# Kernel tuning notes

Hardware: AMD Instinct MI355X
Metric: run time of the kernel (lower is better)

## Reference

```python
import jax, jax.numpy as jnp
import numpy as np

B, P, N, E = 4, 4, 4096, 512
QKV_DIM, HEADS = 512, 8
DH = QKV_DIM // HEADS
EPS = 1e-12  # F.normalize default eps


def setup_inputs() -> dict:
    key = jax.random.key(0)
    ks = jax.random.split(key, 5)
    s = 1.0 / np.sqrt(E)
    return {
        "x": jax.random.normal(ks[0], (B, P, N, E), dtype=jnp.float32),
        "w_qkv": jax.random.normal(ks[1], (3 * QKV_DIM, E), dtype=jnp.float32) * s,
        "b_qkv": jax.random.normal(ks[2], (3 * QKV_DIM,), dtype=jnp.float32) * 0.01,
        "temperature": jnp.ones((HEADS, 1, 1), dtype=jnp.float32),
        "w_out": jax.random.normal(ks[3], (E, QKV_DIM), dtype=jnp.float32) * (1.0 / np.sqrt(QKV_DIM)),
        "b_out": jax.random.normal(ks[4], (E,), dtype=jnp.float32) * 0.01,
    }


def _l2norm(t):
    # F.normalize(t, dim=-1): t / max(||t||_2, eps)
    n = jnp.sqrt(jnp.sum(t * t, axis=-1, keepdims=True))
    return t / jnp.maximum(n, EPS)


def reference(x, w_qkv, b_qkv, temperature, w_out, b_out):
    b, p, n, _ = x.shape
    qkv = x @ w_qkv.T + b_qkv                      # (b,p,n,3*qkv)
    q, k, v = jnp.split(qkv, 3, axis=-1)
    def to_heads(t):
        # (b,p,n,h*dh) -> (b,p,h,dh,n)  (channels-as-tokens)
        t = t.reshape(b, p, n, HEADS, DH)
        return jnp.transpose(t, (0, 1, 3, 4, 2))
    q, k, v = to_heads(q), to_heads(k), to_heads(v)
    q = _l2norm(q)                                  # normalize over tokens n
    k = _l2norm(k)
    # channel-wise (dh x dh) attention per head, temperature-scaled
    attn = jnp.einsum('bphdn,bphen->bphde', q, k) * temperature  # (b,p,h,dh,dh)
    attn = jax.nn.softmax(attn, axis=-1)
    out = jnp.einsum('bphde,bphen->bphdn', attn, v)               # (b,p,h,dh,n)
    # torch rearrange 'b p h n d -> b p d (h n)' on (b,p,h,dh,n) -> (b,p,n,h*dh)
    out = jnp.transpose(out, (0, 1, 4, 2, 3)).reshape(b, p, n, HEADS * DH)
    return out @ w_out.T + b_out
```

## Files before the change

### kernel.cpp

```cpp
#include <hip/hip_runtime.h>
#include <stdint.h>

typedef unsigned short u16;
typedef __bf16 bf16x8 __attribute__((ext_vector_type(8)));
typedef float f32x4 __attribute__((ext_vector_type(4)));

#define AS1 __attribute__((address_space(1)))
#define AS3 __attribute__((address_space(3)))

__device__ __forceinline__ void gload_lds16(u16* lds_wave_base, const u16* g) {
  __builtin_amdgcn_global_load_lds((AS1 void*)g, (AS3 void*)lds_wave_base, 16, 0, 0);
}

__device__ __forceinline__ u16 f2bf(float f) {
  unsigned int u = __float_as_uint(f);
  u += 0x7fffu + ((u >> 16) & 1u);
  return (u16)(u >> 16);
}
__device__ __forceinline__ float bf2f(u16 h) { return __uint_as_float(((unsigned)h) << 16); }

__global__ void cast_f32_bf16(const float* __restrict__ in, u16* __restrict__ out, int n8) {
  int i = blockIdx.x * blockDim.x + threadIdx.x;
  if (i >= n8) return;
  const float4* p = (const float4*)in + (size_t)i * 2;
  float4 a = p[0], b = p[1];
  uint2 lo, hi;
  lo.x = (unsigned)f2bf(a.x) | ((unsigned)f2bf(a.y) << 16);
  lo.y = (unsigned)f2bf(a.z) | ((unsigned)f2bf(a.w) << 16);
  hi.x = (unsigned)f2bf(b.x) | ((unsigned)f2bf(b.y) << 16);
  hi.y = (unsigned)f2bf(b.z) | ((unsigned)f2bf(b.w) << 16);
  uint2* o = (uint2*)out + (size_t)i * 2;
  o[0] = lo;
  o[1] = hi;
}

__global__ __launch_bounds__(256) void cast_x(const float* __restrict__ x,
                                              u16* __restrict__ xbf,
                                              float* __restrict__ svec) {
  __shared__ float sred[4 * 512];
  const int b = blockIdx.x;
  const int bp = b >> 6;
  const int n0 = (b & 63) * 64;
  const int t = threadIdx.x;
  const int e8 = (t & 63) * 8;
  const int r0 = t >> 6;
  const float* xb = x + ((size_t)(bp * 4096 + n0) * 512) + e8;
  u16* ob = xbf + ((size_t)(bp * 4096 + n0) * 512) + e8;
  float s0 = 0.f, s1 = 0.f, s2 = 0.f, s3 = 0.f, s4 = 0.f, s5 = 0.f, s6 = 0.f, s7 = 0.f;
#pragma unroll 2
  for (int pass = 0; pass < 16; ++pass) {
    const int r = pass * 4 + r0;
    const float* p = xb + (size_t)r * 512;
    float4 v0 = *(const float4*)p;
    float4 v1 = *(const float4*)(p + 4);
    uint2 lo, hi;
    lo.x = (unsigned)f2bf(v0.x) | ((unsigned)f2bf(v0.y) << 16);
    lo.y = (unsigned)f2bf(v0.z) | ((unsigned)f2bf(v0.w) << 16);
    hi.x = (unsigned)f2bf(v1.x) | ((unsigned)f2bf(v1.y) << 16);
    hi.y = (unsigned)f2bf(v1.z) | ((unsigned)f2bf(v1.w) << 16);
    uint2* o = (uint2*)(ob + (size_t)r * 512);
    o[0] = lo;
    o[1] = hi;
    s0 += v0.x; s1 += v0.y; s2 += v0.z; s3 += v0.w;
    s4 += v1.x; s5 += v1.y; s6 += v1.z; s7 += v1.w;
  }
  float* sp = &sred[r0 * 512 + e8];
  sp[0] = s0; sp[1] = s1; sp[2] = s2; sp[3] = s3;
  sp[4] = s4; sp[5] = s5; sp[6] = s6; sp[7] = s7;
  __syncthreads();
  {
    const int e = t * 2;
    float a0 = sred[e] + sred[512 + e] + sred[1024 + e] + sred[1536 + e];
    float a1 = sred[e + 1] + sred[512 + e + 1] + sred[1024 + e + 1] + sred[1536 + e + 1];
    float* sv = svec + (size_t)bp * 512 + e;
    atomicAdd(sv + 0, a0);
    atomicAdd(sv + 1, a1);
  }
}

__global__ __launch_bounds__(256) void transpose_x(const u16* __restrict__ xbf,
                                                   u16* __restrict__ xbfT) {
  __shared__ __align__(16) unsigned sm[128 * 36];
  const int b = blockIdx.x;
  const int bp = b >> 8;
  const int tt = (b >> 2) & 63;
  const int et = b & 3;
  const int t = threadIdx.x;
  const int n0 = tt * 64, e0 = et * 128;
  const int c4 = (t & 31) * 4;
  const int pr = t >> 5;
  const int sw1 = t & 15;
  const u16* ib = xbf + ((size_t)(bp * 4096 + n0) * 512) + e0 + c4;
  uint2 ta[4], tb[4];
#pragma unroll
  for (int jp = 0; jp < 4; ++jp) {
    const int n = (jp * 8 + pr) * 2;
    ta[jp] = *(const uint2*)(ib + (size_t)n * 512);
    tb[jp] = *(const uint2*)(ib + (size_t)(n + 1) * 512);
  }
#pragma unroll
  for (int jp = 0; jp < 4; ++jp) {
    const int npair = jp * 8 + pr;
    const uint2 a = ta[jp], v = tb[jp];
    const int col = (npair & 16) | ((npair ^ sw1) & 15);
    sm[(c4 + 0) * 36 + col] = (a.x & 0xFFFFu) | (v.x << 16);
    sm[(c4 + 1) * 36 + col] = (a.x >> 16) | (v.x & 0xFFFF0000u);
    sm[(c4 + 2) * 36 + col] = (a.y & 0xFFFFu) | (v.y << 16);
    sm[(c4 + 3) * 36 + col] = (a.y >> 16) | (v.y & 0xFFFF0000u);
  }
  __syncthreads();
  u16* otb = xbfT + ((size_t)bp * 512 + e0) * 4096 + n0;
#pragma unroll
  for (int it = 0; it < 4; ++it) {
    const int e = it * 32 + (t >> 3);
    const int g = t & 7;
    const int p4 = g * 4;
    const int sw = (e >> 2) & 15;
    const int base = e * 36 + (p4 & 16) + ((p4 ^ sw) & 12);
    uint4 v = *(const uint4*)&sm[base];
    const int s3 = sw & 3;
    unsigned q0 = v.x, q1 = v.y, q2 = v.z, q3 = v.w;
    if (s3 & 1) {
      unsigned tmp = q0; q0 = q1; q1 = tmp;
      tmp = q2; q2 = q3; q3 = tmp;
    }
    if (s3 & 2) {
      unsigned tmp = q0; q0 = q2; q2 = tmp;
      tmp = q1; q1 = q3; q3 = tmp;
    }
    uint4 o;
    o.x = q0; o.y = q1; o.z = q2; o.w = q3;
    *(uint4*)(otb + (size_t)e * 4096 + g * 8) = o;
  }
}

__global__ __launch_bounds__(256) void transpose_wv(const float* __restrict__ wv,
                                                    u16* __restrict__ wvT) {
  __shared__ __align__(16) u16 sm[128 * 136];
  const int b = blockIdx.x;
  const int r0 = (b >> 2) * 128;
  const int c0 = (b & 3) * 128;
  const int t = threadIdx.x;
  const int rsub = t >> 5, c4 = (t & 31) * 4;
#pragma unroll
  for (int j = 0; j < 16; ++j) {
    const int r = j * 8 + rsub;
    float4 v = *(const float4*)(wv + (size_t)(r0 + r) * 512 + c0 + c4);
    sm[(c4 + 0) * 136 + ((j ^ ((c4 + 0) & 15)) << 3) + rsub] = f2bf(v.x);
    sm[(c4 + 1) * 136 + ((j ^ ((c4 + 1) & 15)) << 3) + rsub] = f2bf(v.y);
    sm[(c4 + 2) * 136 + ((j ^ ((c4 + 2) & 15)) << 3) + rsub] = f2bf(v.z);
    sm[(c4 + 3) * 136 + ((j ^ ((c4 + 3) & 15)) << 3) + rsub] = f2bf(v.w);
  }
  __syncthreads();
#pragma unroll
  for (int j = 0; j < 8; ++j) {
    const int re = j * 16 + (t >> 4);
    const int ct8 = t & 15;
    uint4 v = *(const uint4*)&sm[re * 136 + ((ct8 ^ (re & 15)) << 3)];
    *(uint4*)(wvT + (size_t)(c0 + re) * 512 + r0 + ct8 * 8) = v;
  }
}

template <int MODE>
__global__ __launch_bounds__(256) void gemm5(const u16* __restrict__ gA,
                                             const u16* __restrict__ gB,
                                             const float* __restrict__ bias,
                                             void* __restrict__ gC) {
  __shared__ __align__(16) u16 smem[128 * 136];
  u16* As = smem;
  u16* Bs = smem + 4096;
  const int t = threadIdx.x;
  const int w = t >> 6, l = t & 63;
  const int lrow = l & 15, quad = l >> 4;
  const int wm = (w >> 1) * 64, wn = (w & 1) * 64;
  int m0, n0, bp = 0, kc = 0;
  if (MODE == 0) {
    const int bx = blockIdx.x;
    bp = blockIdx.y;
    kc = bx & 3;
    const int p = bx >> 2;
    int ti, tj;
    if (p < 4) { ti = 0; tj = p; }
    else if (p < 7) { ti = 1; tj = p - 3; }
    else if (p < 9) { ti = 2; tj = p - 5; }
    else { ti = 3; tj = 3; }
    m0 = ti * 128;
    n0 = tj * 128;
  } else if (MODE == 1) {
    const int b = blockIdx.x;
    bp = b >> 5;
    const int tl = b & 31;
    m0 = (tl >> 2) * 128;
    n0 = (tl & 3) * 128;
  } else if (MODE == 2) {
    const int b = blockIdx.x;
    bp = b >> 4;
    const int tl = b & 15;
    m0 = (tl >> 2) * 128;
    n0 = (tl & 3) * 128;
  } else {
    const int b = blockIdx.x;
    const int local = b & 127;
    bp = b >> 7;
    const int j = (local >> 3) & 3;
    const int T = ((local >> 5) << 3) | (local & 7);
    m0 = j * 128;
    n0 = T * 128;
  }
  constexpr int LDA = (MODE == 0) ? 4096 : 512;
  constexpr int LDB = (MODE == 0) ? 4096 : 512;
  const u16* pA = gA;
  const u16* pB = gB;
  if (MODE == 0) {
    pA += (size_t)bp * (512 * 4096);
    pB = pA;
  } else if (MODE == 1) {
    pB += (size_t)bp * (512 * 512);
  } else if (MODE == 2) {
    pA += (size_t)bp * (512 * 512);
  } else {
    pA += (size_t)bp * (512 * 512);
    pB += (size_t)bp * (4096 * 512);
  }
  const int srow = w * 32 + (l >> 2);
  const int scol = (l & 3) * 8;
  const int koff = (MODE == 0) ? kc * 1024 : 0;
  const u16* ga0 = pA + (size_t)(m0 + srow) * LDA + scol + koff;
  const u16* ga1 = ga0 + (size_t)16 * LDA;
  const u16* gb0 = pB + (size_t)(n0 + srow) * LDB + scol + koff;
  const u16* gb1 = gb0 + (size_t)16 * LDB;
  u16* lA0 = &As[w * 1024];
  u16* lA1 = lA0 + 512;
  u16* lB0 = &Bs[w * 1024];
  u16* lB1 = lB0 + 512;

  f32x4 acc[4][4];
#pragma unroll
  for (int mi = 0; mi < 4; ++mi)
#pragma unroll
    for (int ni = 0; ni < 4; ++ni) acc[mi][ni] = (f32x4){0.f, 0.f, 0.f, 0.f};

  constexpr int KLEN = (MODE == 0) ? 1024 : 512;
  constexpr int NPH = (MODE == 1) ? 2 : 1;
#pragma unroll 1
  for (int ph = 0; ph < NPH; ++ph) {
    const size_t boff = (MODE == 1) ? (size_t)ph * 4194304 : 0;
#pragma unroll 1
    for (int k0 = 0; k0 < KLEN; k0 += 32) {
      gload_lds16(lA0, ga0 + k0);
      gload_lds16(lA1, ga1 + k0);
      gload_lds16(lB0, gb0 + boff + k0);
      gload_lds16(lB1, gb1 + boff + k0);
      __syncthreads();
      bf16x8 af[4], bfr[4];
#pragma unroll
      for (int mi = 0; mi < 4; ++mi)
        af[mi] = *(const bf16x8*)&As[(wm + mi * 16 + lrow) * 32 + quad * 8];
#pragma unroll
      for (int ni = 0; ni < 4; ++ni)
        bfr[ni] = *(const bf16x8*)&Bs[(wn + ni * 16 + lrow) * 32 + quad * 8];
#pragma unroll
      for (int mi = 0; mi < 4; ++mi)
#pragma unroll
        for (int ni = 0; ni < 4; ++ni)
          acc[mi][ni] = __builtin_amdgcn_mfma_f32_16x16x32_bf16(af[mi], bfr[ni], acc[mi][ni], 0, 0, 0);
      __syncthreads();
    }
  }

  if (MODE == 0 || MODE == 3) {
    float* gCp;
    if (MODE == 0)
      gCp = (float*)gC + (size_t)(kc * 16 + bp) * 262144;
    else
      gCp = (float*)gC + (size_t)bp * (4096 * 512);
    float* fs = (float*)smem;
#pragma unroll
    for (int half = 0; half < 2; ++half) {
      if (half) __syncthreads();
#pragma unroll
      for (int mi = 0; mi < 4; ++mi) {
        const int mrow_l = wm + mi * 16 + quad * 4;
        float4 bb = {0.f, 0.f, 0.f, 0.f};
        if (MODE == 3) bb = *(const float4*)&bias[(size_t)bp * 512 + m0 + mrow_l];
#pragma unroll
        for (int ni = 0; ni < 4; ++ni) {
          const int ncol_l = wn + ni * 16 + lrow;
          if ((ncol_l >> 6) != half) continue;
          f32x4 v = acc[mi][ni];
          float4 o;
          o.x = v[0] + bb.x;
          o.y = v[1] + bb.y;
          o.z = v[2] + bb.z;
          o.w = v[3] + bb.w;
          *(float4*)&fs[(ncol_l & 63) * 136 + mrow_l] = o;
        }
      }
      __syncthreads();
#pragma unroll
      for (int j2 = 0; j2 < 4; ++j2) {
        const int g = j2 * 256 + t;
        const int r = g >> 4;
        const int c = (g & 15) * 8;
        float4 v0 = *(const float4*)&fs[r * 136 + c];
        float4 v1 = *(const float4*)&fs[r * 136 + c + 4];
        float* yp = gCp + ((size_t)(n0 + half * 64 + r) * 512 + m0 + c);
        *(float4*)yp = v0;
        *(float4*)(yp + 4) = v1;
      }
      if (MODE == 0 && m0 != n0) {
#pragma unroll
        for (int j2 = 0; j2 < 8; ++j2) {
          const int g = j2 * 256 + t;
          const int row = g >> 4;
          const int cg = (g & 15) * 4;
          float4 o;
          o.x = fs[(cg + 0) * 136 + row];
          o.y = fs[(cg + 1) * 136 + row];
          o.z = fs[(cg + 2) * 136 + row];
          o.w = fs[(cg + 3) * 136 + row];
          *(float4*)(gCp + (size_t)(m0 + row) * 512 + n0 + half * 64 + cg) = o;
        }
      }
    }
  } else {
    u16* gCp = (u16*)gC + ((MODE == 1) ? (size_t)bp * 524288 : (size_t)bp * 262144);
#pragma unroll
    for (int mi = 0; mi < 4; ++mi) {
      const int mrow_l = wm + mi * 16 + quad * 4;
#pragma unroll
      for (int ni = 0; ni < 4; ++ni) {
        const int ncol_l = wn + ni * 16 + lrow;
        f32x4 v = acc[mi][ni];
        smem[(mrow_l + 0) * 136 + ncol_l] = f2bf(v[0]);
        smem[(mrow_l + 1) * 136 + ncol_l] = f2bf(v[1]);
        smem[(mrow_l + 2) * 136 + ncol_l] = f2bf(v[2]);
        smem[(mrow_l + 3) * 136 + ncol_l] = f2bf(v[3]);
      }
    }
    __syncthreads();
#pragma unroll
    for (int j = 0; j < 8; ++j) {
      const int g = j * 256 + t;
      const int r = g >> 4;
      const int c = (g & 15) * 8;
      uint4 val = *(const uint4*)&smem[r * 136 + c];
      *(uint4*)(gCp + (size_t)(m0 + r) * 512 + n0 + c) = val;
    }
  }
}

__global__ __launch_bounds__(256) void s4red(const float* __restrict__ Spart,
                                             u16* __restrict__ Shi) {
  const size_t i = ((size_t)blockIdx.x * 256 + threadIdx.x) * 4;
  if (i >= 4194304) return;
  float4 a = *(const float4*)(Spart + i);
  float4 b = *(const float4*)(Spart + 4194304 + i);
  float4 c = *(const float4*)(Spart + 2 * 4194304 + i);
  float4 d = *(const float4*)(Spart + 3 * 4194304 + i);
  float s0 = a.x + b.x + c.x + d.x;
  float s1 = a.y + b.y + c.y + d.y;
  float s2 = a.z + b.z + c.z + d.z;
  float s3 = a.w + b.w + c.w + d.w;
  u16 h0 = f2bf(s0), h1 = f2bf(s1), h2 = f2bf(s2), h3 = f2bf(s3);
  uint2 hp;
  hp.x = (unsigned)h0 | ((unsigned)h1 << 16);
  hp.y = (unsigned)h2 | ((unsigned)h3 << 16);
  *(uint2*)(Shi + i) = hp;
  uint2 lp;
  lp.x = (unsigned)f2bf(s0 - bf2f(h0)) | ((unsigned)f2bf(s1 - bf2f(h1)) << 16);
  lp.y = (unsigned)f2bf(s2 - bf2f(h2)) | ((unsigned)f2bf(s3 - bf2f(h3)) << 16);
  *(uint2*)(Shi + 4194304 + i) = lp;
}

__device__ __forceinline__ void bf8_expand(uint4 v, float* o) {
  o[0] = bf2f((u16)(v.x & 0xffff)); o[1] = bf2f((u16)(v.x >> 16));
  o[2] = bf2f((u16)(v.y & 0xffff)); o[3] = bf2f((u16)(v.y >> 16));
  o[4] = bf2f((u16)(v.z & 0xffff)); o[5] = bf2f((u16)(v.z >> 16));
  o[6] = bf2f((u16)(v.w & 0xffff)); o[7] = bf2f((u16)(v.w >> 16));
}

__global__ __launch_bounds__(512) void softmax_weff2(const u16* __restrict__ P,
                                                     const u16* __restrict__ wqkv,
                                                     const float* __restrict__ b_qkv,
                                                     const float* __restrict__ svec,
                                                     const float* __restrict__ temperature,
                                                     const u16* __restrict__ wout,
                                                     u16* __restrict__ Weff) {
  __shared__ __align__(16) float sattn[64 * 64];
  __shared__ __align__(16) u16 sattnT[64 * 64];
  __shared__ float ub[128], dq[128], rnA[128], bb[128];
  const int blk = blockIdx.x;
  const int bp = blk >> 3, h = blk & 7;
  const int t = threadIdx.x, w = t >> 6, l = t & 63;
  const int lrow = l & 15, quad = l >> 4;

  {
    const int mi = w >> 1;
    const int nip = (w & 1) * 2;
    const u16* arow = P + ((size_t)bp * 1024 + h * 64 + mi * 16 + lrow) * 512;
    const u16* brow0 = wqkv + ((size_t)(512 + h * 64 + nip * 16 + lrow)) * 512;
    const u16* brow1 = brow0 + 16 * 512;
    f32x4 c0 = (f32x4){0.f, 0.f, 0.f, 0.f};
    f32x4 c1 = (f32x4){0.f, 0.f, 0.f, 0.f};
#pragma unroll 1
    for (int ks = 0; ks < 16; ++ks) {
      const int ko = ks * 32 + quad * 8;
      bf16x8 a = *(const bf16x8*)(arow + ko);
      bf16x8 b0 = *(const bf16x8*)(brow0 + ko);
      bf16x8 b1 = *(const bf16x8*)(brow1 + ko);
      c0 = __builtin_amdgcn_mfma_f32_16x16x32_bf16(a, b0, c0, 0, 0, 0);
      c1 = __builtin_amdgcn_mfma_f32_16x16x32_bf16(a, b1, c1, 0, 0, 0);
    }
    const int drow = mi * 16 + quad * 4;
#pragma unroll
    for (int r = 0; r < 4; ++r) {
      sattn[(drow + r) * 64 + nip * 16 + lrow] = c0[r];
      sattn[(drow + r) * 64 + (nip + 1) * 16 + lrow] = c1[r];
    }
  }

  {
    const int rr = t >> 2, sub = t & 3;
    const int c = (rr < 64) ? (h * 64 + rr) : (512 + h * 64 + (rr - 64));
    const u16* prow = P + ((size_t)bp * 1024 + c) * 512 + sub * 128;
    const u16* wrow = wqkv + (size_t)c * 512 + sub * 128;
    const float* sv = svec + (size_t)bp * 512 + sub * 128;
    float accp = 0.f, accu = 0.f;
#pragma unroll 1
    for (int i = 0; i < 128; i += 8) {
      float pf[8], wf[8];
      bf8_expand(*(const uint4*)(prow + i), pf);
      bf8_expand(*(const uint4*)(wrow + i), wf);
      float4 s0 = *(const float4*)(sv + i);
      float4 s1 = *(const float4*)(sv + i + 4);
      accp += pf[0] * wf[0] + pf[1] * wf[1] + pf[2] * wf[2] + pf[3] * wf[3] +
              pf[4] * wf[4] + pf[5] * wf[5] + pf[6] * wf[6] + pf[7] * wf[7];
      accu += wf[0] * s0.x + wf[1] * s0.y + wf[2] * s0.z + wf[3] * s0.w +
              wf[4] * s1.x + wf[5] * s1.y + wf[6] * s1.z + wf[7] * s1.w;
    }
    accp += __shfl_xor(accp, 1);
    accp += __shfl_xor(accp, 2);
    accu += __shfl_xor(accu, 1);
    accu += __shfl_xor(accu, 2);
    if (sub == 0) {
      dq[rr] = accp;
      ub[rr] = accu;
    }
  }
  __syncthreads();

  if (t < 128) {
    const int c = (t < 64) ? (h * 64 + t) : (512 + h * 64 + (t - 64));
    const float bc = b_qkv[c];
    const float ss = dq[t] + 2.f * bc * ub[t] + 4096.f * bc * bc;
    rnA[t] = 1.f / fmaxf(sqrtf(ss), 1e-12f);
    bb[t] = bc;
  }
  __syncthreads();

  if (t < 64) {
    const int d = t;
    const float rq = rnA[d], uqv = ub[d], bq = bb[d];
    const float tmp = temperature[h];
    float mx = -1e30f;
    for (int e = 0; e < 64; ++e) {
      const int idx = (e + d) & 63;
      const float bk = bb[64 + idx];
      float g = sattn[d * 64 + idx] + bq * ub[64 + idx] + bk * uqv + 4096.f * bq * bk;
      float v = g * rq * rnA[64 + idx] * tmp;
      sattn[d * 64 + idx] = v;
      mx = fmaxf(mx, v);
    }
    float s = 0.f;
    for (int e = 0; e < 64; ++e) {
      const int idx = (e + d) & 63;
      float p = __expf(sattn[d * 64 + idx] - mx);
      s += p;
      sattn[d * 64 + idx] = p;
    }
    const float inv = 1.f / s;
    for (int e = 0; e < 64; ++e) {
      const int idx = (e + d) & 63;
      sattnT[idx * 64 + d] = f2bf(sattn[d * 64 + idx] * inv);
    }
  }
  __syncthreads();

  bf16x8 a0[4], a1[4];
#pragma unroll
  for (int mi = 0; mi < 4; ++mi) {
    a0[mi] = *(const bf16x8*)&sattnT[(mi * 16 + lrow) * 64 + quad * 8];
    a1[mi] = *(const bf16x8*)&sattnT[(mi * 16 + lrow) * 64 + 32 + quad * 8];
  }
  u16* wb = Weff + ((size_t)bp * (512 * 512));
#pragma unroll 1
  for (int nb = 0; nb < 4; ++nb) {
    const int co = (w * 4 + nb) * 16 + lrow;
    const u16* wrow = wout + (size_t)co * 512 + h * 64;
    bf16x8 b0 = *(const bf16x8*)(wrow + quad * 8);
    bf16x8 b1 = *(const bf16x8*)(wrow + 32 + quad * 8);
#pragma unroll
    for (int mi = 0; mi < 4; ++mi) {
      f32x4 c = (f32x4){0.f, 0.f, 0.f, 0.f};
      c = __builtin_amdgcn_mfma_f32_16x16x32_bf16(a0[mi], b0, c, 0, 0, 0);
      c = __builtin_amdgcn_mfma_f32_16x16x32_bf16(a1[mi], b1, c, 0, 0, 0);
      const int e0 = mi * 16 + quad * 4;
      uint2 pk;
      pk.x = (unsigned)f2bf(c[0]) | ((unsigned)f2bf(c[1]) << 16);
      pk.y = (unsigned)f2bf(c[2]) | ((unsigned)f2bf(c[3]) << 16);
      *(uint2*)(wb + (size_t)co * 512 + h * 64 + e0) = pk;
    }
  }
}

__global__ __launch_bounds__(512) void yb_kernel(const u16* __restrict__ Weff,
                                                 const float* __restrict__ b_qkv,
                                                 const float* __restrict__ b_out,
                                                 float* __restrict__ yb) {
  const int bp = blockIdx.x, co = threadIdx.x;
  const u16* wr = Weff + ((size_t)bp * 512 + co) * 512;
  float s = b_out[co];
#pragma unroll 1
  for (int i = 0; i < 512; i += 8) {
    float wf[8];
    bf8_expand(*(const uint4*)(wr + i), wf);
    const float4 b0 = *(const float4*)(b_qkv + 1024 + i);
    const float4 b1 = *(const float4*)(b_qkv + 1024 + i + 4);
    s += wf[0] * b0.x + wf[1] * b0.y + wf[2] * b0.z + wf[3] * b0.w +
         wf[4] * b1.x + wf[5] * b1.y + wf[6] * b1.z + wf[7] * b1.w;
  }
  yb[(size_t)bp * 512 + co] = s;
}

extern "C" void kernel_launch(void* const* d_in, const int* in_sizes, int n_in,
                              void* d_out, int out_size, void* d_ws, size_t ws_size,
                              hipStream_t stream) {
  const float* x = (const float*)d_in[0];
  const float* w_qkv = (const float*)d_in[1];
  const float* b_qkv = (const float*)d_in[2];
  const float* temp = (const float*)d_in[3];
  const float* w_out = (const float*)d_in[4];
  const float* b_out = (const float*)d_in[5];
  float* y = (float*)d_out;

  char* ws = (char*)d_ws;
  u16* x_bf = (u16*)(ws);
  u16* x_bfT = (u16*)(ws + 67108864);
  u16* wqkv_bf = (u16*)(ws + 134217728);
  u16* wout_bf = (u16*)(ws + 135790592);
  u16* wvT_bf = (u16*)(ws + 136314880);
  u16* S_hi = (u16*)(ws + 136839168);
  u16* P_bf = (u16*)(ws + 153616384);
  u16* Weff = (u16*)(ws + 170393600);
  u16* M_bf = (u16*)(ws + 178782208);
  float* svec = (float*)(ws + 187170816);
  float* yb = (float*)(ws + 187203584);
  float* Spart = (float*)(ws + 187236352);

  hipMemsetAsync(svec, 0, 32768, stream);
  cast_x<<<1024, 256, 0, stream>>>(x, x_bf, svec);
  transpose_x<<<4096, 256, 0, stream>>>(x_bf, x_bfT);
  cast_f32_bf16<<<384, 256, 0, stream>>>(w_qkv, wqkv_bf, 786432 / 8);
  cast_f32_bf16<<<128, 256, 0, stream>>>(w_out, wout_bf, 262144 / 8);
  transpose_wv<<<16, 256, 0, stream>>>(w_qkv + 1024 * 512, wvT_bf);
  gemm5<0><<<dim3(40, 16), 256, 0, stream>>>(x_bfT, x_bfT, nullptr, Spart);
  s4red<<<4096, 256, 0, stream>>>(Spart, S_hi);
  gemm5<1><<<512, 256, 0, stream>>>(wqkv_bf, S_hi, nullptr, P_bf);
  softmax_weff2<<<128, 512, 0, stream>>>(P_bf, wqkv_bf, b_qkv, svec, temp, wout_bf, Weff);
  yb_kernel<<<16, 512, 0, stream>>>(Weff, b_qkv, b_out, yb);
  gemm5<2><<<256, 256, 0, stream>>>(Weff, wvT_bf, nullptr, M_bf);
  gemm5<3><<<2048, 256, 0, stream>>>(M_bf, x_bf, yb, y);
}
```

Before: 519.0 us.

## Process two K-chunks per sync in gemm5 and use nontemporal float stores

```diff
diff --git a/kernel.cpp b/kernel.cpp
--- a/kernel.cpp
+++ b/kernel.cpp
@@ -4,6 +4,7 @@
 typedef unsigned short u16;
 typedef __bf16 bf16x8 __attribute__((ext_vector_type(8)));
 typedef float f32x4 __attribute__((ext_vector_type(4)));
+typedef float f4v __attribute__((ext_vector_type(4)));
 
 #define AS1 __attribute__((address_space(1)))
 #define AS3 __attribute__((address_space(3)))
@@ -18,6 +19,12 @@
   return (u16)(u >> 16);
 }
 __device__ __forceinline__ float bf2f(u16 h) { return __uint_as_float(((unsigned)h) << 16); }
+
+__device__ __forceinline__ void nt_store_f4(float* p, float a, float b, float c, float d) {
+  f4v v;
+  v[0] = a; v[1] = b; v[2] = c; v[3] = d;
+  __builtin_nontemporal_store(v, (f4v*)p);
+}
 
 __global__ void cast_f32_bf16(const float* __restrict__ in, u16* __restrict__ out, int n8) {
   int i = blockIdx.x * blockDim.x + threadIdx.x;
@@ -167,8 +174,10 @@
                                              const float* __restrict__ bias,
                                              void* __restrict__ gC) {
   __shared__ __align__(16) u16 smem[128 * 136];
-  u16* As = smem;
-  u16* Bs = smem + 4096;
+  u16* As0 = smem;
+  u16* As1 = smem + 4096;
+  u16* Bs0 = smem + 8192;
+  u16* Bs1 = smem + 12288;
   const int t = threadIdx.x;
   const int w = t >> 6, l = t & 63;
   const int lrow = l & 15, quad = l >> 4;
@@ -229,10 +238,14 @@
   const u16* ga1 = ga0 + (size_t)16 * LDA;
   const u16* gb0 = pB + (size_t)(n0 + srow) * LDB + scol + koff;
   const u16* gb1 = gb0 + (size_t)16 * LDB;
-  u16* lA0 = &As[w * 1024];
-  u16* lA1 = lA0 + 512;
-  u16* lB0 = &Bs[w * 1024];
-  u16* lB1 = lB0 + 512;
+  u16* lA0a = &As0[w * 1024];
+  u16* lA0b = lA0a + 512;
+  u16* lA1a = &As1[w * 1024];
+  u16* lA1b = lA1a + 512;
+  u16* lB0a = &Bs0[w * 1024];
+  u16* lB0b = lB0a + 512;
+  u16* lB1a = &Bs1[w * 1024];
+  u16* lB1b = lB1a + 512;
 
   f32x4 acc[4][4];
 #pragma unroll
@@ -246,24 +259,45 @@
   for (int ph = 0; ph < NPH; ++ph) {
     const size_t boff = (MODE == 1) ? (size_t)ph * 4194304 : 0;
 #pragma unroll 1
-    for (int k0 = 0; k0 < KLEN; k0 += 32) {
-      gload_lds16(lA0, ga0 + k0);
-      gload_lds16(lA1, ga1 + k0);
-      gload_lds16(lB0, gb0 + boff + k0);
-      gload_lds16(lB1, gb1 + boff + k0);
+    for (int k0 = 0; k0 < KLEN; k0 += 64) {
+      gload_lds16(lA0a, ga0 + k0);
+      gload_lds16(lA0b, ga1 + k0);
+      gload_lds16(lA1a, ga0 + k0 + 32);
+      gload_lds16(lA1b, ga1 + k0 + 32);
+      gload_lds16(lB0a, gb0 + boff + k0);
+      gload_lds16(lB0b, gb1 + boff + k0);
+      gload_lds16(lB1a, gb0 + boff + k0 + 32);
+      gload_lds16(lB1b, gb1 + boff + k0 + 32);
       __syncthreads();
-      bf16x8 af[4], bfr[4];
-#pragma unroll
-      for (int mi = 0; mi < 4; ++mi)
-        af[mi] = *(const bf16x8*)&As[(wm + mi * 16 + lrow) * 32 + quad * 8];
-#pragma unroll
-      for (int ni = 0; ni < 4; ++ni)
-        bfr[ni] = *(const bf16x8*)&Bs[(wn + ni * 16 + lrow) * 32 + quad * 8];
-#pragma unroll
-      for (int mi = 0; mi < 4; ++mi)
+      {
+        bf16x8 af[4], bfr[4];
+#pragma unroll
+        for (int mi = 0; mi < 4; ++mi)
+          af[mi] = *(const bf16x8*)&As0[(wm + mi * 16 + lrow) * 32 + quad * 8];
 #pragma unroll
         for (int ni = 0; ni < 4; ++ni)
-          acc[mi][ni] = __builtin_amdgcn_mfma_f32_16x16x32_bf16(af[mi], bfr[ni], acc[mi][ni], 0, 0, 0);
+          bfr[ni] = *(const bf16x8*)&Bs0[(wn + ni * 16 + lrow) * 32 + quad * 8];
+#pragma unroll
+        for (int mi = 0; mi < 4; ++mi)
+#pragma unroll
+          for (int ni = 0; ni < 4; ++ni)
+            acc[mi][ni] = __builtin_amdgcn_mfma_f32_16x16x32_bf16(af[mi], bfr[ni], acc[mi][ni], 0, 0, 0);
+      }
+      __builtin_amdgcn_sched_barrier(0);
+      {
+        bf16x8 af[4], bfr[4];
+#pragma unroll
+        for (int mi = 0; mi < 4; ++mi)
+          af[mi] = *(const bf16x8*)&As1[(wm + mi * 16 + lrow) * 32 + quad * 8];
+#pragma unroll
+        for (int ni = 0; ni < 4; ++ni)
+          bfr[ni] = *(const bf16x8*)&Bs1[(wn + ni * 16 + lrow) * 32 + quad * 8];
+#pragma unroll
+        for (int mi = 0; mi < 4; ++mi)
+#pragma unroll
+          for (int ni = 0; ni < 4; ++ni)
+            acc[mi][ni] = __builtin_amdgcn_mfma_f32_16x16x32_bf16(af[mi], bfr[ni], acc[mi][ni], 0, 0, 0);
+      }
       __syncthreads();
     }
   }
@@ -305,8 +339,8 @@
         float4 v0 = *(const float4*)&fs[r * 136 + c];
         float4 v1 = *(const float4*)&fs[r * 136 + c + 4];
         float* yp = gCp + ((size_t)(n0 + half * 64 + r) * 512 + m0 + c);
-        *(float4*)yp = v0;
-        *(float4*)(yp + 4) = v1;
+        nt_store_f4(yp, v0.x, v0.y, v0.z, v0.w);
+        nt_store_f4(yp + 4, v1.x, v1.y, v1.z, v1.w);
       }
       if (MODE == 0 && m0 != n0) {
 #pragma unroll
@@ -314,12 +348,9 @@
           const int g = j2 * 256 + t;
           const int row = g >> 4;
           const int cg = (g & 15) * 4;
-          float4 o;
-          o.x = fs[(cg + 0) * 136 + row];
-          o.y = fs[(cg + 1) * 136 + row];
-          o.z = fs[(cg + 2) * 136 + row];
-          o.w = fs[(cg + 3) * 136 + row];
-          *(float4*)(gCp + (size_t)(m0 + row) * 512 + n0 + half * 64 + cg) = o;
+          nt_store_f4(gCp + (size_t)(m0 + row) * 512 + n0 + half * 64 + cg,
+                      fs[(cg + 0) * 136 + row], fs[(cg + 1) * 136 + row],
+                      fs[(cg + 2) * 136 + row], fs[(cg + 3) * 136 + row]);
         }
       }
     }
```

Result: no change. 523.0 us (+0.8%).
